# Performance work log

Hardware: AMD Instinct MI355X
Metric: run time of the kernel (lower is better)

## Reference

```python
import jax, jax.numpy as jnp
import numpy as np

NV, NC, E, D = 100000, 400000, 1600000, 128

def _mlp2(x, w1, b1, w2, b2):
    # Linear->ReLU->Linear->ReLU (weights stored [in, out])
    return jax.nn.relu(jax.nn.relu(x @ w1 + b1) @ w2 + b2)

def setup_inputs() -> dict:
    key = jax.random.key(0)
    ks = jax.random.split(key, 16)
    s = 1.0 / np.sqrt(D)
    return {
        "hv": jax.random.normal(ks[0], (NV, D), jnp.float32),
        "hc": jax.random.normal(ks[1], (NC, D), jnp.float32),
        "row_v": jax.random.randint(ks[2], (E,), 0, NV, jnp.int32),
        "col_v": jax.random.randint(ks[3], (E,), 0, 2 * NC, jnp.int32),
        "row_c": jax.random.randint(ks[4], (E,), 0, NC, jnp.int32),
        "col_c": jax.random.randint(ks[5], (E,), 0, 2 * NV, jnp.int32),
        # message MLPs: order [fmv_pos, fmv_neg, fmc_pos, fmc_neg]
        "mw1": jax.random.normal(ks[6], (4, D, D), jnp.float32) * s,
        "mb1": jax.random.normal(ks[7], (4, D), jnp.float32) * s,
        "mw2": jax.random.normal(ks[8], (4, D, D), jnp.float32) * s,
        "mb2": jax.random.normal(ks[9], (4, D), jnp.float32) * s,
        # update MLPs: order [fuv, fuc]; first layer takes concat(h, m) -> 2D in
        "uw1": jax.random.normal(ks[10], (2, 2 * D, D), jnp.float32) * s,
        "ub1": jax.random.normal(ks[11], (2, D), jnp.float32) * s,
        "uw2": jax.random.normal(ks[12], (2, D, D), jnp.float32) * s,
        "ub2": jax.random.normal(ks[13], (2, D), jnp.float32) * s,
    }

def reference(hv, hc, row_v, col_v, row_c, col_c,
              mw1, mb1, mw2, mb2, uw1, ub1, uw2, ub2):
    nv, nc = hv.shape[0], hc.shape[0]
    # message: transform clause feats with pos/neg MLPs, concat rows, spmm via gather+segment_sum
    zv = jnp.concatenate([
        _mlp2(hc, mw1[0], mb1[0], mw2[0], mb2[0]),  # fmv_pos(hc)
        _mlp2(hc, mw1[1], mb1[1], mw2[1], mb2[1]),  # fmv_neg(hc)
    ], axis=0)                                       # [2*NC, D]
    mv = jax.ops.segment_sum(zv[col_v], row_v, num_segments=nv)  # spmm(vadj, zv)
    zc = jnp.concatenate([
        _mlp2(hv, mw1[2], mb1[2], mw2[2], mb2[2]),  # fmc_pos(hv)
        _mlp2(hv, mw1[3], mb1[3], mw2[3], mb2[3]),  # fmc_neg(hv)
    ], axis=0)                                       # [2*NV, D]
    mc = jax.ops.segment_sum(zc[col_c], row_c, num_segments=nc)  # spmm(cadj, zc)
    # update: concat(h, m) -> MLP
    hv_new = _mlp2(jnp.concatenate([hv, mv], axis=1), uw1[0], ub1[0], uw2[0], ub2[0])
    hc_new = _mlp2(jnp.concatenate([hc, mc], axis=1), uw1[1], ub1[1], uw2[1], ub2[1])
    return (hv_new, hc_new)
```

## Files before the change

kernel.cpp:

```cpp
#include <hip/hip_runtime.h>
#include <hip/hip_bf16.h>

#define NVV 100000
#define NCC 400000
#define NEE 1600000

typedef short short8 __attribute__((ext_vector_type(8)));
typedef short short4v __attribute__((ext_vector_type(4)));
typedef float f32x4 __attribute__((ext_vector_type(4)));
typedef unsigned int u32x2 __attribute__((ext_vector_type(2)));
typedef unsigned int u32x4 __attribute__((ext_vector_type(4)));

__device__ __forceinline__ float b2f(short s) {
    unsigned int u = ((unsigned int)(unsigned short)s) << 16;
    return __builtin_bit_cast(float, u);
}
__device__ __forceinline__ short f2b(float f) {
    __hip_bfloat16 h = __float2bfloat16(f);
    return __builtin_bit_cast(short, h);
}
__device__ __forceinline__ unsigned int cvtpk(float a, float b) {
    unsigned int r;
    asm("v_cvt_pk_bf16_f32 %0, %1, %2" : "=v"(r) : "v"(a), "v"(b));
    return r;
}

__global__ __launch_bounds__(256)
void prep_all(const float* __restrict__ mw1, const float* __restrict__ mw2,
              const float* __restrict__ uw1, const float* __restrict__ uw2,
              short* __restrict__ wt_m1, short* __restrict__ wt_m2,
              short* __restrict__ wt_u1, short* __restrict__ wt_u2)
{
    int e = blockIdx.x * 256 + threadIdx.x;
    const float* W; short* WT; int K; int idx;
    if (e < 65536)        { W = mw1; WT = wt_m1; K = 128; idx = e; }
    else if (e < 131072)  { W = mw2; WT = wt_m2; K = 128; idx = e - 65536; }
    else if (e < 196608)  { W = uw1; WT = wt_u1; K = 256; idx = e - 131072; }
    else if (e < 229376)  { W = uw2; WT = wt_u2; K = 128; idx = e - 196608; }
    else return;
    int mk = idx >> 7, n = idx & 127;
    int mi = mk / K, k = mk - mi * K;
    WT[(size_t)mi * K * 128 + (size_t)n * K + k] = f2b(W[idx]);
}

__global__ __launch_bounds__(256)
void to_bf16_2(const float* __restrict__ hv, const float* __restrict__ hc,
               short* __restrict__ hvb, short* __restrict__ hcb)
{
    const long nv = (long)NVV * 128;
    const long nc = (long)NCC * 128;
    long i0 = ((long)blockIdx.x * 256 + threadIdx.x) * 8;
    long stride = (long)gridDim.x * 256 * 8;
    for (long i = i0; i < nv + nc; i += stride) {
        const float* in; short* outp; long j;
        if (i < nv) { in = hv; outp = hvb; j = i; }
        else        { in = hc; outp = hcb; j = i - nv; }
        f32x4 a = *(const f32x4*)(in + j);
        f32x4 b = *(const f32x4*)(in + j + 4);
        u32x4 o;
        o[0] = cvtpk(a[0], a[1]);
        o[1] = cvtpk(a[2], a[3]);
        o[2] = cvtpk(b[0], b[1]);
        o[3] = cvtpk(b[2], b[3]);
        *(u32x4*)(outp + j) = o;
    }
}

template<int NW>
__global__ __launch_bounds__(NW * 64, 1)
void mlp2_msg_ws(const short* __restrict__ Xb,
                 const short* __restrict__ W1T, const float* __restrict__ B1,
                 const short* __restrict__ W2T, const float* __restrict__ B2,
                 short* __restrict__ Z, size_t zstr, int M, int nChunks)
{
    constexpr int BM = NW * 32;
    constexpr int NT = NW * 64;
    __shared__ short sW1[128 * 136];
    __shared__ short sW2[128 * 136];
    __shared__ short sH[BM * 136];

    const int tid = threadIdx.x;
    const int lane = tid & 63;
    const int w = tid >> 6;
    const int p = lane & 15;
    const int q = lane >> 4;

    const int set = blockIdx.x & 1;
    const int c0 = blockIdx.x >> 1;
    const int cstr = gridDim.x >> 1;

    const short* w1g = W1T + set * 16384;
    const short* w2g = W2T + set * 16384;
    const float* b1g = B1 + set * 128;
    const float* b2g = B2 + set * 128;
    short* z = Z + (size_t)set * zstr;

    for (int e = tid * 8; e < 128 * 128; e += NT * 8) {
        int n = e >> 7, k = e & 127;
        *(short8*)(sW1 + n * 136 + k) = *(const short8*)(w1g + e);
        *(short8*)(sW2 + n * 136 + k) = *(const short8*)(w2g + e);
    }
    __syncthreads();

    if (c0 >= nChunks) return;

    short8 xfA[2][4], xfB[2][4];

    auto issueX = [&](short8 (&xf)[2][4], int c) {
        long base = (long)c * BM + w * 32;
        #pragma unroll
        for (int t = 0; t < 2; ++t) {
            long m = base + t * 16 + p;
            if (m > (long)M - 1) m = (long)M - 1;
            const short* src = Xb + m * 128 + q * 8;
            #pragma unroll
            for (int kk = 0; kk < 4; ++kk)
                xf[t][kk] = *(const short8*)(src + kk * 32);
        }
    };

    auto computeStore = [&](short8 (&xf)[2][4], int c) {
        long base = (long)c * BM + w * 32;
        f32x4 acc[8][2];
        #pragma unroll
        for (int cc = 0; cc < 8; ++cc)
            #pragma unroll
            for (int t = 0; t < 2; ++t)
                acc[cc][t] = (f32x4){0.f, 0.f, 0.f, 0.f};

        #pragma unroll
        for (int kk = 0; kk < 4; ++kk) {
            short8 af[8];
            #pragma unroll
            for (int cc = 0; cc < 8; ++cc)
                af[cc] = *(const short8*)(sW1 + (cc * 16 + p) * 136 + kk * 32 + q * 8);
            #pragma unroll
            for (int cc = 0; cc < 8; ++cc)
                #pragma unroll
                for (int t = 0; t < 2; ++t)
                    acc[cc][t] = __builtin_amdgcn_mfma_f32_16x16x32_bf16(af[cc], xf[t][kk], acc[cc][t], 0, 0, 0);
        }

        #pragma unroll
        for (int cc = 0; cc < 8; ++cc) {
            f32x4 bb = *(const f32x4*)(b1g + cc * 16 + q * 4);
            #pragma unroll
            for (int t = 0; t < 2; ++t) {
                u32x2 u;
                u[0] = cvtpk(fmaxf(acc[cc][t][0] + bb[0], 0.f), fmaxf(acc[cc][t][1] + bb[1], 0.f));
                u[1] = cvtpk(fmaxf(acc[cc][t][2] + bb[2], 0.f), fmaxf(acc[cc][t][3] + bb[3], 0.f));
                *(u32x2*)(sH + (w * 32 + t * 16 + p) * 136 + cc * 16 + q * 4) = u;
            }
        }
        asm volatile("s_waitcnt lgkmcnt(0)" ::: "memory");

        f32x4 acc2[8][2];
        #pragma unroll
        for (int cc = 0; cc < 8; ++cc)
            #pragma unroll
            for (int t = 0; t < 2; ++t)
                acc2[cc][t] = (f32x4){0.f, 0.f, 0.f, 0.f};

        #pragma unroll
        for (int kk = 0; kk < 4; ++kk) {
            short8 af[8], bfr[2];
            #pragma unroll
            for (int cc = 0; cc < 8; ++cc)
                af[cc] = *(const short8*)(sW2 + (cc * 16 + p) * 136 + kk * 32 + q * 8);
            #pragma unroll
            for (int t = 0; t < 2; ++t)
                bfr[t] = *(const short8*)(sH + (w * 32 + t * 16 + p) * 136 + kk * 32 + q * 8);
            #pragma unroll
            for (int cc = 0; cc < 8; ++cc)
                #pragma unroll
                for (int t = 0; t < 2; ++t)
                    acc2[cc][t] = __builtin_amdgcn_mfma_f32_16x16x32_bf16(af[cc], bfr[t], acc2[cc][t], 0, 0, 0);
        }

        #pragma unroll
        for (int cc = 0; cc < 8; ++cc) {
            f32x4 bb = *(const f32x4*)(b2g + cc * 16 + q * 4);
            #pragma unroll
            for (int t = 0; t < 2; ++t) {
                long m = base + t * 16 + p;
                if (m < M) {
                    u32x2 u;
                    u[0] = cvtpk(fmaxf(acc2[cc][t][0] + bb[0], 0.f), fmaxf(acc2[cc][t][1] + bb[1], 0.f));
                    u[1] = cvtpk(fmaxf(acc2[cc][t][2] + bb[2], 0.f), fmaxf(acc2[cc][t][3] + bb[3], 0.f));
                    *(u32x2*)(z + m * 128 + cc * 16 + q * 4) = u;
                }
            }
        }
    };

    int c = c0;
    issueX(xfA, c);
    while (true) {
        if (c + cstr < nChunks) issueX(xfB, c + cstr);
        computeStore(xfA, c);
        c += cstr; if (c >= nChunks) break;
        if (c + cstr < nChunks) issueX(xfA, c + cstr);
        computeStore(xfB, c);
        c += cstr; if (c >= nChunks) break;
    }
}

template<int NW>
__global__ __launch_bounds__(NW * 64, 1)
void mlp2_upd_fused(const short* __restrict__ Xb, const short* __restrict__ z,
                    const int* __restrict__ offs, const int* __restrict__ edgeCol,
                    const short* __restrict__ W1T, const float* __restrict__ B1,
                    const short* __restrict__ W2T, const float* __restrict__ B2,
                    float* __restrict__ Out, int M, int nChunks)
{
    constexpr int BM = NW * 32;
    constexpr int NT = NW * 64;
    __shared__ short sW1[128 * 264];
    __shared__ short sW2[128 * 136];
    __shared__ short sH[BM * 136];

    const int tid = threadIdx.x;
    const int lane = tid & 63;
    const int w = tid >> 6;
    const int p = lane & 15;
    const int q = lane >> 4;

    const int c0 = blockIdx.x;
    const int cstr = gridDim.x;

    for (int e = tid * 8; e < 128 * 256; e += NT * 8) {
        int n = e >> 8, k = e & 255;
        *(short8*)(sW1 + n * 264 + k) = *(const short8*)(W1T + e);
    }
    for (int e = tid * 8; e < 128 * 128; e += NT * 8) {
        int n = e >> 7, k = e & 127;
        *(short8*)(sW2 + n * 136 + k) = *(const short8*)(W2T + e);
    }
    __syncthreads();

    if (c0 >= nChunks) return;

    short8 dA[2][4], dB[2][4];

    auto issueDense = [&](short8 (&d)[2][4], int c) {
        long base = (long)c * BM + w * 32;
        #pragma unroll
        for (int t = 0; t < 2; ++t) {
            long m = base + t * 16 + p;
            if (m > (long)M - 1) m = (long)M - 1;
            const short* s1 = Xb + m * 128 + q * 8;
            #pragma unroll
            for (int kk = 0; kk < 4; ++kk)
                d[t][kk] = *(const short8*)(s1 + kk * 32);
        }
    };

    auto computeStore = [&](short8 (&d)[2][4], int c, bool pre, short8 (&dn)[2][4], int cn) {
        long base = (long)c * BM + w * 32;

        short8 gx[2][4];
        #pragma unroll
        for (int t = 0; t < 2; ++t) {
            long m = base + t * 16 + p;
            if (m > (long)M - 1) m = (long)M - 1;
            float a[4][8];
            #pragma unroll
            for (int kk = 0; kk < 4; ++kk)
                #pragma unroll
                for (int i = 0; i < 8; ++i) a[kk][i] = 0.f;

            int beg = offs[m], end = offs[m + 1];
            int j = beg;
            for (; j + 1 < end; j += 2) {
                int e0 = edgeCol[j], e1 = edgeCol[j + 1];
                #pragma unroll
                for (int kk = 0; kk < 4; ++kk) {
                    short8 v0 = *(const short8*)(z + (long)e0 * 128 + kk * 32 + q * 8);
                    short8 v1 = *(const short8*)(z + (long)e1 * 128 + kk * 32 + q * 8);
                    #pragma unroll
                    for (int i = 0; i < 8; ++i)
                        a[kk][i] += b2f(v0[i]) + b2f(v1[i]);
                }
            }
            if (j < end) {
                int e0 = edgeCol[j];
                #pragma unroll
                for (int kk = 0; kk < 4; ++kk) {
                    short8 v0 = *(const short8*)(z + (long)e0 * 128 + kk * 32 + q * 8);
                    #pragma unroll
                    for (int i = 0; i < 8; ++i) a[kk][i] += b2f(v0[i]);
                }
            }
            #pragma unroll
            for (int kk = 0; kk < 4; ++kk) {
                u32x4 o;
                o[0] = cvtpk(a[kk][0], a[kk][1]);
                o[1] = cvtpk(a[kk][2], a[kk][3]);
                o[2] = cvtpk(a[kk][4], a[kk][5]);
                o[3] = cvtpk(a[kk][6], a[kk][7]);
                gx[t][kk] = __builtin_bit_cast(short8, o);
            }
        }

        if (pre) issueDense(dn, cn);

        f32x4 acc[8][2];
        #pragma unroll
        for (int cc = 0; cc < 8; ++cc)
            #pragma unroll
            for (int t = 0; t < 2; ++t)
                acc[cc][t] = (f32x4){0.f, 0.f, 0.f, 0.f};

        #pragma unroll
        for (int kk = 0; kk < 8; ++kk) {
            short8 af[8];
            #pragma unroll
            for (int cc = 0; cc < 8; ++cc)
                af[cc] = *(const short8*)(sW1 + (cc * 16 + p) * 264 + kk * 32 + q * 8);
            #pragma unroll
            for (int cc = 0; cc < 8; ++cc)
                #pragma unroll
                for (int t = 0; t < 2; ++t) {
                    short8 xcur = (kk < 4) ? d[t][kk] : gx[t][kk - 4];
                    acc[cc][t] = __builtin_amdgcn_mfma_f32_16x16x32_bf16(af[cc], xcur, acc[cc][t], 0, 0, 0);
                }
        }

        #pragma unroll
        for (int cc = 0; cc < 8; ++cc) {
            f32x4 bb = *(const f32x4*)(B1 + cc * 16 + q * 4);
            #pragma unroll
            for (int t = 0; t < 2; ++t) {
                u32x2 u;
                u[0] = cvtpk(fmaxf(acc[cc][t][0] + bb[0], 0.f), fmaxf(acc[cc][t][1] + bb[1], 0.f));
                u[1] = cvtpk(fmaxf(acc[cc][t][2] + bb[2], 0.f), fmaxf(acc[cc][t][3] + bb[3], 0.f));
                *(u32x2*)(sH + (w * 32 + t * 16 + p) * 136 + cc * 16 + q * 4) = u;
            }
        }
        asm volatile("s_waitcnt lgkmcnt(0)" ::: "memory");

        f32x4 acc2[8][2];
        #pragma unroll
        for (int cc = 0; cc < 8; ++cc)
            #pragma unroll
            for (int t = 0; t < 2; ++t)
                acc2[cc][t] = (f32x4){0.f, 0.f, 0.f, 0.f};

        #pragma unroll
        for (int kk = 0; kk < 4; ++kk) {
            short8 af[8], bfr[2];
            #pragma unroll
            for (int cc = 0; cc < 8; ++cc)
                af[cc] = *(const short8*)(sW2 + (cc * 16 + p) * 136 + kk * 32 + q * 8);
            #pragma unroll
            for (int t = 0; t < 2; ++t)
                bfr[t] = *(const short8*)(sH + (w * 32 + t * 16 + p) * 136 + kk * 32 + q * 8);
            #pragma unroll
            for (int cc = 0; cc < 8; ++cc)
                #pragma unroll
                for (int t = 0; t < 2; ++t)
                    acc2[cc][t] = __builtin_amdgcn_mfma_f32_16x16x32_bf16(af[cc], bfr[t], acc2[cc][t], 0, 0, 0);
        }

        #pragma unroll
        for (int cc = 0; cc < 8; ++cc) {
            f32x4 bb = *(const f32x4*)(B2 + cc * 16 + q * 4);
            #pragma unroll
            for (int t = 0; t < 2; ++t) {
                long m = base + t * 16 + p;
                if (m < M) {
                    f32x4 fv;
                    #pragma unroll
                    for (int i = 0; i < 4; ++i)
                        fv[i] = fmaxf(acc2[cc][t][i] + bb[i], 0.f);
                    *(f32x4*)(Out + m * 128 + cc * 16 + q * 4) = fv;
                }
            }
        }
    };

    int c = c0;
    issueDense(dA, c);
    while (true) {
        computeStore(dA, c, c + cstr < nChunks, dB, c + cstr);
        c += cstr; if (c >= nChunks) break;
        computeStore(dB, c, c + cstr < nChunks, dA, c + cstr);
        c += cstr; if (c >= nChunks) break;
    }
}


__global__ __launch_bounds__(256)
void hist2(const int* __restrict__ row_v, const int* __restrict__ row_c,
           int* __restrict__ cnt_v, int* __restrict__ cnt_c)
{
    int e = blockIdx.x * 256 + threadIdx.x;
    if (e < NEE) atomicAdd(&cnt_v[row_v[e]], 1);
    else if (e < 2 * NEE) atomicAdd(&cnt_c[row_c[e - NEE]], 1);
}

__global__ __launch_bounds__(256)
void seg_reduce2(const int* __restrict__ cnt_v, const int* __restrict__ cnt_c,
                 int* __restrict__ bsum_v, int* __restrict__ bsum_c, int Bv)
{
    __shared__ int s[256];
    int b = blockIdx.x, t = threadIdx.x;
    const int* counts; int* bsum; int N; int bb;
    if (b < Bv) { counts = cnt_v; bsum = bsum_v; N = NVV; bb = b; }
    else        { counts = cnt_c; bsum = bsum_c; N = NCC; bb = b - Bv; }
    int base = bb * 512;
    int v = 0;
    if (base + t < N) v += counts[base + t];
    if (base + 256 + t < N) v += counts[base + 256 + t];
    s[t] = v;
    __syncthreads();
    for (int off = 128; off > 0; off >>= 1) {
        if (t < off) s[t] += s[t + off];
        __syncthreads();
    }
    if (t == 0) bsum[bb] = s[0];
}

__global__ __launch_bounds__(1024)
void scan_bsum2(int* __restrict__ bsum_v, int* __restrict__ bsum_c, int Bv, int Bc)
{
    __shared__ int s[1024];
    int* bsum = (blockIdx.x == 0) ? bsum_v : bsum_c;
    int B = (blockIdx.x == 0) ? Bv : Bc;
    int t = threadIdx.x;
    s[t] = (t < B) ? bsum[t] : 0;
    __syncthreads();
    for (int off = 1; off < 1024; off <<= 1) {
        int v = (t >= off) ? s[t - off] : 0;
        __syncthreads();
        s[t] += v;
        __syncthreads();
    }
    if (t < B) bsum[t] = (t == 0) ? 0 : s[t - 1];
}

__global__ __launch_bounds__(512)
void scan_final2(const int* __restrict__ cnt_v, const int* __restrict__ cnt_c,
                 const int* __restrict__ bsum_v, const int* __restrict__ bsum_c,
                 int* __restrict__ offs_v, int* __restrict__ offs_c, int Bv)
{
    __shared__ int s[512];
    int b = blockIdx.x, t = threadIdx.x;
    const int* counts; const int* bsum; int* offs; int N; int bb;
    if (b < Bv) { counts = cnt_v; bsum = bsum_v; offs = offs_v; N = NVV; bb = b; }
    else        { counts = cnt_c; bsum = bsum_c; offs = offs_c; N = NCC; bb = b - Bv; }
    int idx = bb * 512 + t;
    int c = (idx < N) ? counts[idx] : 0;
    s[t] = c;
    __syncthreads();
    for (int off = 1; off < 512; off <<= 1) {
        int v = (t >= off) ? s[t - off] : 0;
        __syncthreads();
        s[t] += v;
        __syncthreads();
    }
    if (idx < N) offs[idx] = bsum[bb] + s[t] - c;
    if (idx == N - 1) offs[N] = bsum[bb] + s[t];
}

__global__ __launch_bounds__(256)
void csr_fill2(const int* __restrict__ row_v, const int* __restrict__ col_v,
               const int* __restrict__ row_c, const int* __restrict__ col_c,
               const int* __restrict__ offs_v, const int* __restrict__ offs_c,
               int* __restrict__ cur_v, int* __restrict__ cur_c,
               int* __restrict__ edge_v, int* __restrict__ edge_c)
{
    int e = blockIdx.x * 256 + threadIdx.x;
    if (e < NEE) {
        int r = row_v[e];
        int pos = offs_v[r] + atomicAdd(&cur_v[r], 1);
        edge_v[pos] = col_v[e];
    } else if (e < 2 * NEE) {
        int ee = e - NEE;
        int r = row_c[ee];
        int pos = offs_c[r] + atomicAdd(&cur_c[r], 1);
        edge_c[pos] = col_c[ee];
    }
}

extern "C" void kernel_launch(void* const* d_in, const int* in_sizes, int n_in,
                              void* d_out, int out_size, void* d_ws, size_t ws_size,
                              hipStream_t stream)
{
    const float* hv   = (const float*)d_in[0];
    const float* hc   = (const float*)d_in[1];
    const int* row_v  = (const int*)d_in[2];
    const int* col_v  = (const int*)d_in[3];
    const int* row_c  = (const int*)d_in[4];
    const int* col_c  = (const int*)d_in[5];
    const float* mw1  = (const float*)d_in[6];
    const float* mb1  = (const float*)d_in[7];
    const float* mw2  = (const float*)d_in[8];
    const float* mb2  = (const float*)d_in[9];
    const float* uw1  = (const float*)d_in[10];
    const float* ub1  = (const float*)d_in[11];
    const float* uw2  = (const float*)d_in[12];
    const float* ub2  = (const float*)d_in[13];
    float* out = (float*)d_out;

    short* zv = (short*)d_ws;
    short* zc = zv + (size_t)2 * NCC * 128;
    short* wt_m1 = zc + (size_t)2 * NVV * 128;
    short* wt_m2 = wt_m1 + 4 * 16384;
    short* wt_u1 = wt_m2 + 4 * 16384;
    short* wt_u2 = wt_u1 + 2 * 32768;
    short* hvb = wt_u2 + 2 * 16384;
    short* hcb = hvb + (size_t)NVV * 128;
    int* edge_v = (int*)(hcb + (size_t)NCC * 128);
    int* edge_c = edge_v + NEE;
    int* offs_v = edge_c + NEE;
    int* offs_c = offs_v + (NVV + 1);
    int* cnt_v  = offs_c + (NCC + 1);
    int* cnt_c  = cnt_v + NVV;
    int* bsum_v = cnt_c + NCC;
    int* bsum_c = bsum_v + 1024;

    const int Bv = (NVV + 511) / 512;
    const int Bc = (NCC + 511) / 512;

    prep_all<<<(229376 + 255) / 256, 256, 0, stream>>>(
        mw1, mw2, uw1, uw2, wt_m1, wt_m2, wt_u1, wt_u2);
    to_bf16_2<<<2048, 256, 0, stream>>>(hv, hc, hvb, hcb);

    hipMemsetAsync(cnt_v, 0, (NVV + NCC) * sizeof(int), stream);
    hist2<<<(2 * NEE + 255) / 256, 256, 0, stream>>>(row_v, row_c, cnt_v, cnt_c);
    seg_reduce2<<<Bv + Bc, 256, 0, stream>>>(cnt_v, cnt_c, bsum_v, bsum_c, Bv);
    scan_bsum2<<<2, 1024, 0, stream>>>(bsum_v, bsum_c, Bv, Bc);
    scan_final2<<<Bv + Bc, 512, 0, stream>>>(cnt_v, cnt_c, bsum_v, bsum_c, offs_v, offs_c, Bv);
    hipMemsetAsync(cnt_v, 0, (NVV + NCC) * sizeof(int), stream);
    csr_fill2<<<(2 * NEE + 255) / 256, 256, 0, stream>>>(
        row_v, col_v, row_c, col_c, offs_v, offs_c, cnt_v, cnt_c, edge_v, edge_c);

    mlp2_msg_ws<8><<<256, 512, 0, stream>>>(
        hcb, wt_m1, mb1, wt_m2, mb2, zv, (size_t)NCC * 128, NCC, (NCC + 255) / 256);
    mlp2_msg_ws<8><<<256, 512, 0, stream>>>(
        hvb, wt_m1 + 2 * 16384, mb1 + 2 * 128, wt_m2 + 2 * 16384, mb2 + 2 * 128,
        zc, (size_t)NVV * 128, NVV, (NVV + 255) / 256);

    mlp2_upd_fused<6><<<256, 384, 0, stream>>>(
        hvb, zv, offs_v, edge_v, wt_u1, ub1, wt_u2, ub2, out, NVV, (NVV + 191) / 192);
    mlp2_upd_fused<6><<<256, 384, 0, stream>>>(
        hcb, zc, offs_c, edge_c, wt_u1 + 32768, ub1 + 128, wt_u2 + 16384, ub2 + 128,
        out + (size_t)NVV * 128, NCC, (NCC + 191) / 192);
}
```

Measured before the change: 1.274 ms.

## Split CSR gather into standalone kernel and merge message/update launches

The sparse gather-sum that lived inside the update MLP kernel moves into a dedicated csr_gather_all kernel. It assigns 16 lanes per row and unrolls edges by four, writing bf16 messages mv/mc to workspace. The two message-MLP launches become one launch with a fixed block split between clause and variable sets, and the two update launches are merged the same way. The update kernel then loads dense h and m and prefetches the next tile, with sched_barrier added. This decouples the irregular gather from the MFMA pipeline and cuts launch count, at the cost of an extra bf16 write and read of the message arrays.

```diff
diff --git a/kernel.cpp b/kernel.cpp
--- a/kernel.cpp
+++ b/kernel.cpp
@@ -68,10 +68,10 @@
 
 template<int NW>
 __global__ __launch_bounds__(NW * 64, 1)
-void mlp2_msg_ws(const short* __restrict__ Xb,
-                 const short* __restrict__ W1T, const float* __restrict__ B1,
-                 const short* __restrict__ W2T, const float* __restrict__ B2,
-                 short* __restrict__ Z, size_t zstr, int M, int nChunks)
+void mlp2_msg_all(const short* __restrict__ hcb, const short* __restrict__ hvb,
+                  const short* __restrict__ WT1, const float* __restrict__ B1a,
+                  const short* __restrict__ WT2, const float* __restrict__ B2a,
+                  short* __restrict__ zv, short* __restrict__ zc, int splitC)
 {
     constexpr int BM = NW * 32;
     constexpr int NT = NW * 64;
@@ -85,15 +85,22 @@
     const int p = lane & 15;
     const int q = lane >> 4;
 
-    const int set = blockIdx.x & 1;
-    const int c0 = blockIdx.x >> 1;
-    const int cstr = gridDim.x >> 1;
-
-    const short* w1g = W1T + set * 16384;
-    const short* w2g = W2T + set * 16384;
-    const float* b1g = B1 + set * 128;
-    const float* b2g = B2 + set * 128;
-    short* z = Z + (size_t)set * zstr;
+    int b = blockIdx.x;
+    const short* X; short* z; int M, c0, cstr, set;
+    if (b < splitC) {
+        set = b & 1; X = hcb; z = zv + (size_t)set * NCC * 128;
+        M = NCC; c0 = b >> 1; cstr = splitC >> 1;
+    } else {
+        int bb = b - splitC;
+        set = 2 + (bb & 1); X = hvb; z = zc + (size_t)(bb & 1) * NVV * 128;
+        M = NVV; c0 = bb >> 1; cstr = (gridDim.x - splitC) >> 1;
+    }
+    const int nChunks = (M + BM - 1) / BM;
+
+    const short* w1g = WT1 + set * 16384;
+    const short* w2g = WT2 + set * 16384;
+    const float* b1g = B1a + set * 128;
+    const float* b2g = B2a + set * 128;
 
     for (int e = tid * 8; e < 128 * 128; e += NT * 8) {
         int n = e >> 7, k = e & 127;
@@ -112,11 +119,12 @@
         for (int t = 0; t < 2; ++t) {
             long m = base + t * 16 + p;
             if (m > (long)M - 1) m = (long)M - 1;
-            const short* src = Xb + m * 128 + q * 8;
+            const short* src = X + m * 128 + q * 8;
             #pragma unroll
             for (int kk = 0; kk < 4; ++kk)
                 xf[t][kk] = *(const short8*)(src + kk * 32);
         }
+        __builtin_amdgcn_sched_barrier(0);
     };
 
     auto computeStore = [&](short8 (&xf)[2][4], int c) {
@@ -207,11 +215,11 @@
 
 template<int NW>
 __global__ __launch_bounds__(NW * 64, 1)
-void mlp2_upd_fused(const short* __restrict__ Xb, const short* __restrict__ z,
-                    const int* __restrict__ offs, const int* __restrict__ edgeCol,
-                    const short* __restrict__ W1T, const float* __restrict__ B1,
-                    const short* __restrict__ W2T, const float* __restrict__ B2,
-                    float* __restrict__ Out, int M, int nChunks)
+void mlp2_upd_all(const short* __restrict__ hvb, const short* __restrict__ hcb,
+                  const short* __restrict__ mv, const short* __restrict__ mc,
+                  const short* __restrict__ wt_u1, const float* __restrict__ ub1,
+                  const short* __restrict__ wt_u2, const float* __restrict__ ub2,
+                  float* __restrict__ out, int splitV)
 {
     constexpr int BM = NW * 32;
     constexpr int NT = NW * 64;
@@ -225,8 +233,20 @@
     const int p = lane & 15;
     const int q = lane >> 4;
 
-    const int c0 = blockIdx.x;
-    const int cstr = gridDim.x;
+    int b = blockIdx.x;
+    const short *X, *X2; float* O; int M, c0, cstr, set;
+    if (b < splitV) {
+        set = 0; X = hvb; X2 = mv; O = out; M = NVV; c0 = b; cstr = splitV;
+    } else {
+        set = 1; X = hcb; X2 = mc; O = out + (size_t)NVV * 128; M = NCC;
+        c0 = b - splitV; cstr = gridDim.x - splitV;
+    }
+    const int nChunks = (M + BM - 1) / BM;
+
+    const short* W1T = wt_u1 + set * 32768;
+    const short* W2T = wt_u2 + set * 16384;
+    const float* B1 = ub1 + set * 128;
+    const float* B2 = ub2 + set * 128;
 
     for (int e = tid * 8; e < 128 * 256; e += NT * 8) {
         int n = e >> 8, k = e & 255;
@@ -240,70 +260,27 @@
 
     if (c0 >= nChunks) return;
 
-    short8 dA[2][4], dB[2][4];
-
-    auto issueDense = [&](short8 (&d)[2][4], int c) {
+    short8 bufA[2][8], bufB[2][8];
+
+    auto issueX = [&](short8 (&xf)[2][8], int c) {
         long base = (long)c * BM + w * 32;
         #pragma unroll
         for (int t = 0; t < 2; ++t) {
             long m = base + t * 16 + p;
             if (m > (long)M - 1) m = (long)M - 1;
-            const short* s1 = Xb + m * 128 + q * 8;
-            #pragma unroll
-            for (int kk = 0; kk < 4; ++kk)
-                d[t][kk] = *(const short8*)(s1 + kk * 32);
-        }
+            const short* s1 = X + m * 128 + q * 8;
+            const short* s2 = X2 + m * 128 + q * 8;
+            #pragma unroll
+            for (int kk = 0; kk < 4; ++kk) {
+                xf[t][kk]     = *(const short8*)(s1 + kk * 32);
+                xf[t][kk + 4] = *(const short8*)(s2 + kk * 32);
+            }
+        }
+        __builtin_amdgcn_sched_barrier(0);
     };
 
-    auto computeStore = [&](short8 (&d)[2][4], int c, bool pre, short8 (&dn)[2][4], int cn) {
+    auto computeStore = [&](short8 (&xf)[2][8], int c) {
         long base = (long)c * BM + w * 32;
-
-        short8 gx[2][4];
-        #pragma unroll
-        for (int t = 0; t < 2; ++t) {
-            long m = base + t * 16 + p;
-            if (m > (long)M - 1) m = (long)M - 1;
-            float a[4][8];
-            #pragma unroll
-            for (int kk = 0; kk < 4; ++kk)
-                #pragma unroll
-                for (int i = 0; i < 8; ++i) a[kk][i] = 0.f;
-
-            int beg = offs[m], end = offs[m + 1];
-            int j = beg;
-            for (; j + 1 < end; j += 2) {
-                int e0 = edgeCol[j], e1 = edgeCol[j + 1];
-                #pragma unroll
-                for (int kk = 0; kk < 4; ++kk) {
-                    short8 v0 = *(const short8*)(z + (long)e0 * 128 + kk * 32 + q * 8);
-                    short8 v1 = *(const short8*)(z + (long)e1 * 128 + kk * 32 + q * 8);
-                    #pragma unroll
-                    for (int i = 0; i < 8; ++i)
-                        a[kk][i] += b2f(v0[i]) + b2f(v1[i]);
-                }
-            }
-            if (j < end) {
-                int e0 = edgeCol[j];
-                #pragma unroll
-                for (int kk = 0; kk < 4; ++kk) {
-                    short8 v0 = *(const short8*)(z + (long)e0 * 128 + kk * 32 + q * 8);
-                    #pragma unroll
-                    for (int i = 0; i < 8; ++i) a[kk][i] += b2f(v0[i]);
-                }
-            }
-            #pragma unroll
-            for (int kk = 0; kk < 4; ++kk) {
-                u32x4 o;
-                o[0] = cvtpk(a[kk][0], a[kk][1]);
-                o[1] = cvtpk(a[kk][2], a[kk][3]);
-                o[2] = cvtpk(a[kk][4], a[kk][5]);
-                o[3] = cvtpk(a[kk][6], a[kk][7]);
-                gx[t][kk] = __builtin_bit_cast(short8, o);
-            }
-        }
-
-        if (pre) issueDense(dn, cn);
-
         f32x4 acc[8][2];
         #pragma unroll
         for (int cc = 0; cc < 8; ++cc)
@@ -320,10 +297,8 @@
             #pragma unroll
             for (int cc = 0; cc < 8; ++cc)
                 #pragma unroll
-                for (int t = 0; t < 2; ++t) {
-                    short8 xcur = (kk < 4) ? d[t][kk] : gx[t][kk - 4];
-                    acc[cc][t] = __builtin_amdgcn_mfma_f32_16x16x32_bf16(af[cc], xcur, acc[cc][t], 0, 0, 0);
-                }
+                for (int t = 0; t < 2; ++t)
+                    acc[cc][t] = __builtin_amdgcn_mfma_f32_16x16x32_bf16(af[cc], xf[t][kk], acc[cc][t], 0, 0, 0);
         }
 
         #pragma unroll
@@ -373,18 +348,20 @@
                     #pragma unroll
                     for (int i = 0; i < 4; ++i)
                         fv[i] = fmaxf(acc2[cc][t][i] + bb[i], 0.f);
-                    *(f32x4*)(Out + m * 128 + cc * 16 + q * 4) = fv;
+                    *(f32x4*)(O + m * 128 + cc * 16 + q * 4) = fv;
                 }
             }
         }
     };
 
     int c = c0;
-    issueDense(dA, c);
+    issueX(bufA, c);
     while (true) {
-        computeStore(dA, c, c + cstr < nChunks, dB, c + cstr);
+        if (c + cstr < nChunks) issueX(bufB, c + cstr);
+        computeStore(bufA, c);
         c += cstr; if (c >= nChunks) break;
-        computeStore(dB, c, c + cstr < nChunks, dA, c + cstr);
+        if (c + cstr < nChunks) issueX(bufA, c + cstr);
+        computeStore(bufB, c);
         c += cstr; if (c >= nChunks) break;
     }
 }
@@ -481,6 +458,55 @@
         int pos = offs_c[r] + atomicAdd(&cur_c[r], 1);
         edge_c[pos] = col_c[ee];
     }
+}
+
+__global__ __launch_bounds__(256)
+void csr_gather_all(const short* __restrict__ zv, const short* __restrict__ zc,
+                    const int* __restrict__ offs_v, const int* __restrict__ edge_v,
+                    const int* __restrict__ offs_c, const int* __restrict__ edge_c,
+                    short* __restrict__ mv, short* __restrict__ mc)
+{
+    int wid = (int)((blockIdx.x * 256 + threadIdx.x) >> 6);
+    int lane = threadIdx.x & 63;
+    int sub = lane >> 4;
+    int sl = lane & 15;
+    int row = wid * 4 + sub;
+    if (row >= NVV + NCC) return;
+
+    const short* z; const int* offs; const int* ec; short* md; int r;
+    if (row < NVV) { z = zv; offs = offs_v; ec = edge_v; md = mv; r = row; }
+    else           { z = zc; offs = offs_c; ec = edge_c; md = mc; r = row - NVV; }
+
+    int beg = offs[r], end = offs[r + 1];
+
+    float a[8];
+    #pragma unroll
+    for (int i = 0; i < 8; ++i) a[i] = 0.f;
+
+    int j = beg;
+    for (; j + 3 < end; j += 4) {
+        int c0 = ec[j], c1 = ec[j + 1], c2 = ec[j + 2], c3 = ec[j + 3];
+        short8 v0 = *(const short8*)(z + (long)c0 * 128 + sl * 8);
+        short8 v1 = *(const short8*)(z + (long)c1 * 128 + sl * 8);
+        short8 v2 = *(const short8*)(z + (long)c2 * 128 + sl * 8);
+        short8 v3 = *(const short8*)(z + (long)c3 * 128 + sl * 8);
+        #pragma unroll
+        for (int i = 0; i < 8; ++i)
+            a[i] += (b2f(v0[i]) + b2f(v1[i])) + (b2f(v2[i]) + b2f(v3[i]));
+    }
+    for (; j < end; ++j) {
+        int c = ec[j];
+        short8 v = *(const short8*)(z + (long)c * 128 + sl * 8);
+        #pragma unroll
+        for (int i = 0; i < 8; ++i) a[i] += b2f(v[i]);
+    }
+
+    u32x4 o;
+    o[0] = cvtpk(a[0], a[1]);
+    o[1] = cvtpk(a[2], a[3]);
+    o[2] = cvtpk(a[4], a[5]);
+    o[3] = cvtpk(a[6], a[7]);
+    *(u32x4*)(md + (long)r * 128 + sl * 8) = o;
 }
 
 extern "C" void kernel_launch(void* const* d_in, const int* in_sizes, int n_in,
@@ -505,7 +531,9 @@
 
     short* zv = (short*)d_ws;
     short* zc = zv + (size_t)2 * NCC * 128;
-    short* wt_m1 = zc + (size_t)2 * NVV * 128;
+    short* mv = zc + (size_t)2 * NVV * 128;
+    short* mc = mv + (size_t)NVV * 128;
+    short* wt_m1 = mc + (size_t)NCC * 128;
     short* wt_m2 = wt_m1 + 4 * 16384;
     short* wt_u1 = wt_m2 + 4 * 16384;
     short* wt_u2 = wt_u1 + 2 * 32768;
@@ -536,15 +564,12 @@
     csr_fill2<<<(2 * NEE + 255) / 256, 256, 0, stream>>>(
         row_v, col_v, row_c, col_c, offs_v, offs_c, cnt_v, cnt_c, edge_v, edge_c);
 
-    mlp2_msg_ws<8><<<256, 512, 0, stream>>>(
-        hcb, wt_m1, mb1, wt_m2, mb2, zv, (size_t)NCC * 128, NCC, (NCC + 255) / 256);
-    mlp2_msg_ws<8><<<256, 512, 0, stream>>>(
-        hvb, wt_m1 + 2 * 16384, mb1 + 2 * 128, wt_m2 + 2 * 16384, mb2 + 2 * 128,
-        zc, (size_t)NVV * 128, NVV, (NVV + 255) / 256);
-
-    mlp2_upd_fused<6><<<256, 384, 0, stream>>>(
-        hvb, zv, offs_v, edge_v, wt_u1, ub1, wt_u2, ub2, out, NVV, (NVV + 191) / 192);
-    mlp2_upd_fused<6><<<256, 384, 0, stream>>>(
-        hcb, zc, offs_c, edge_c, wt_u1 + 32768, ub1 + 128, wt_u2 + 16384, ub2 + 128,
-        out + (size_t)NVV * 128, NCC, (NCC + 191) / 192);
-}
+    mlp2_msg_all<8><<<256, 512, 0, stream>>>(
+        hcb, hvb, wt_m1, mb1, wt_m2, mb2, zv, zc, 204);
+
+    csr_gather_all<<<((NVV + NCC) / 4 + 3) / 4, 256, 0, stream>>>(
+        zv, zc, offs_v, edge_v, offs_c, edge_c, mv, mc);
+
+    mlp2_upd_all<6><<<256, 384, 0, stream>>>(
+        hvb, hcb, mv, mc, wt_u1, ub1, wt_u2, ub2, out, 51);
+}
```

After: 1.187 ms. 6.9% less time.
